# Kernel optimization log

Measured on AMD Instinct MI355X. Metric: run time of the kernel, lower is better.

Reference implementation:

```python
import jax, jax.numpy as jnp
import numpy as np

B, C, H, W = 2, 4, 256, 256   # x shape; H == W == num_classes
NH = 2                         # num_heads
NC = 256                       # num_classes
CT = C * 256                   # conv output channels (dim * 16 * 16)
NCR = NC // 16                 # MLP reduced dim


def setup_inputs() -> dict:
    key = jax.random.key(0)
    ks = jax.random.split(key, 16)
    s = 0.02

    def n(k, shape):
        return jax.random.normal(k, shape, jnp.float32) * s

    inp = {
        "x": jax.random.normal(ks[0], (B, C, H, W), jnp.float32),
        "conv_w": n(ks[1], (CT, C, 3, 3)),          # OIHW
        "conv_b": jnp.zeros((CT,), jnp.float32),
        # MLP weights stored (in, out) so y = x @ W + b  (== torch Linear)
        "qW1": n(ks[2], (NC, NCR)), "qb1": jnp.zeros((NCR,), jnp.float32),
        "qW2": n(ks[3], (NC, NCR)), "qb2": jnp.zeros((NCR,), jnp.float32),
        "kW1": n(ks[4], (NC, NCR)), "kb1": jnp.zeros((NCR,), jnp.float32),
        "kW2": n(ks[5], (NC, NCR)), "kb2": jnp.zeros((NCR,), jnp.float32),
        "vW1": n(ks[6], (NC, NCR)), "vb1": jnp.zeros((NCR,), jnp.float32),
        "vW2": n(ks[7], (NC, NCR)), "vb2": jnp.zeros((NCR,), jnp.float32),
        "temperature": jnp.ones((NH * NH, 1, 1), jnp.float32),
    }
    return inp


def _mlp(x, W1, b1, W2, b2):
    # Linear+sigmoid on last dim (w), transpose, Linear+sigmoid on (h), transpose back
    x = jax.nn.sigmoid(x @ W1 + b1)      # (b, ct, h, w//16)
    x = jnp.swapaxes(x, 2, 3)            # (b, ct, w//16, h)
    x = jax.nn.sigmoid(x @ W2 + b2)      # (b, ct, w//16, h//16)
    return jnp.swapaxes(x, 2, 3)         # (b, ct, h//16, w//16)


def _to_heads(a, nh):
    # einops: 'b c (h head1) (w head2) -> b (head1 head2) c (h w)'
    bb, ct, ht, wt = a.shape
    a = a.reshape(bb, ct, ht // nh, nh, wt // nh, nh)
    a = a.transpose(0, 3, 5, 1, 2, 4)    # (b, head1, head2, c, h, w)
    return a.reshape(bb, nh * nh, ct, (ht // nh) * (wt // nh))


def reference(x, conv_w, conv_b, qW1, qb1, qW2, qb2, kW1, kb1, kW2, kb2,
              vW1, vb1, vW2, vb2, temperature):
    b, c, h, w = x.shape
    t = jax.lax.conv_general_dilated(
        x, conv_w, window_strides=(1, 1), padding=((1, 1), (1, 1)),
        dimension_numbers=("NCHW", "OIHW", "NCHW")) + conv_b[None, :, None, None]
    q = _to_heads(_mlp(t, qW1, qb1, qW2, qb2), NH)   # (b, nh^2, ct, hw')
    k = _to_heads(_mlp(t, kW1, kb1, kW2, kb2), NH)
    v = _to_heads(_mlp(t, vW1, vb1, vW2, vb2), NH)
    scores = jnp.einsum('bncx,bnex->bnce', q, k) * temperature  # (b, nh^2, ct, ct)
    p = jax.nn.softmax(scores, axis=-1)
    att = jnp.einsum('bnce,bnex->bncx', p, v)                   # (b, nh^2, ct, hw')
    return att.reshape(b, c, h, w)
```

## Files before the change

### kernel.cpp

```cpp
#include <hip/hip_runtime.h>
#include <cstdint>

constexpr int NB  = 2;
constexpr int NCI = 4;
constexpr int NHH = 256;
constexpr int NWW = 256;
constexpr int NCT = 1024;

constexpr size_t SW1F = 0;
constexpr size_t U16_BASE_F = 48;
constexpr size_t GP_U  = 0;
constexpr size_t CW_U  = 297216;
constexpr size_t W2T_U = 338176;
constexpr size_t QU_O  = 350464;
constexpr size_t KU_O  = 874752;
constexpr size_t VT_O  = 1399040;

typedef __attribute__((ext_vector_type(8))) short bf16x8;
typedef __attribute__((ext_vector_type(4))) float f32x4;

__device__ __forceinline__ uint16_t f2bf(float x) {
  uint32_t u = __float_as_uint(x);
  return (uint16_t)((u + 0x7FFFu + ((u >> 16) & 1u)) >> 16);
}
__device__ __forceinline__ uint32_t pk2bf(float a, float b) {
  const uint32_t au = __float_as_uint(a) + 0x8000u;
  const uint32_t bu = __float_as_uint(b) + 0x8000u;
  return __builtin_amdgcn_perm(bu, au, 0x07060302u);
}
__device__ __forceinline__ float sigmoid_f(float v) {
  return __builtin_amdgcn_rcpf(1.0f + __expf(-v));
}

__global__ __launch_bounds__(64) void k1_G(
    const float* __restrict__ x,
    const float* __restrict__ qW1, const float* __restrict__ kW1,
    const float* __restrict__ vW1,
    const float* __restrict__ conv_w,
    const float* __restrict__ qW2, const float* __restrict__ kW2,
    const float* __restrict__ vW2,
    float* __restrict__ wsf, uint16_t* __restrict__ wsu) {
  const int tid = threadIdx.x;
  const int NBLK = 3 * NB * NCI * (NHH / 4);
  int bid = blockIdx.x;

  if (bid >= NBLK + 3 + 64) {
    const int p = bid - (NBLK + 3 + 64);
    const int m = p >> 3;
    const int h0 = (p & 7) * 32;
    const float* W2 = (m == 0) ? qW2 : (m == 1) ? kW2 : vW2;
    const int hh = tid >> 1, part = tid & 1;
    const float* src = W2 + (size_t)(h0 + hh) * 16 + part * 8;
    const float4 a = *(const float4*)(src);
    const float4 b2 = *(const float4*)(src + 4);
    uint16_t* dst = wsu + W2T_U + (size_t)m * 4096 + h0 + hh;
    dst[(part * 8 + 0) * 256] = f2bf(a.x);
    dst[(part * 8 + 1) * 256] = f2bf(a.y);
    dst[(part * 8 + 2) * 256] = f2bf(a.z);
    dst[(part * 8 + 3) * 256] = f2bf(a.w);
    dst[(part * 8 + 4) * 256] = f2bf(b2.x);
    dst[(part * 8 + 5) * 256] = f2bf(b2.y);
    dst[(part * 8 + 6) * 256] = f2bf(b2.z);
    dst[(part * 8 + 7) * 256] = f2bf(b2.w);
    return;
  }
  if (bid >= NBLK + 3) {
    const int p = bid - (NBLK + 3);
    const int o = p * 16 + (tid >> 2);
    const int ks = (tid & 3) * 10;
    for (int u = 0; u < 10; ++u) {
      const int k = ks + u;
      wsu[CW_U + (size_t)o * 40 + k] = (k < 36) ? f2bf(conv_w[o * 36 + k]) : (uint16_t)0;
    }
    return;
  }
  if (bid >= NBLK) {
    const int m = bid - NBLK;
    const float* W1 = (m == 0) ? qW1 : (m == 1) ? kW1 : vW1;
    const int wc = tid >> 4, r = tid & 15;
    float s = 0.f;
    #pragma unroll 8
    for (int i = 0; i < 64; ++i) s += W1[(wc * 64 + i) * 16 + r];
    s += __shfl_xor(s, 16, 64);
    s += __shfl_xor(s, 32, 64);
    if (tid < 16) wsf[SW1F + m * 16 + tid] = s;
    return;
  }

  const int m  = bid / (NB * NCI * (NHH / 4));
  int rem      = bid % (NB * NCI * (NHH / 4));
  const int b  = rem / (NCI * (NHH / 4));
  rem          = rem % (NCI * (NHH / 4));
  const int i  = rem / (NHH / 4);
  const int h0 = (rem % (NHH / 4)) * 4;
  const int mb = m * NB + b;

  const float* W1 = (m == 0) ? qW1 : (m == 1) ? kW1 : vW1;

  __shared__ float W1l[16 * 260];
  __shared__ float xlb[4][260];

  for (int idx4 = tid; idx4 < 1024; idx4 += 64) {
    const float4 t = ((const float4*)W1)[idx4];
    const int w = idx4 >> 2, r0 = (idx4 & 3) * 4;
    W1l[(r0 + 0) * 260 + w] = t.x;
    W1l[(r0 + 1) * 260 + w] = t.y;
    W1l[(r0 + 2) * 260 + w] = t.z;
    W1l[(r0 + 3) * 260 + w] = t.w;
  }
  const float* xbase = x + ((size_t)(b * NCI + i) * NHH + h0) * NWW;
  for (int idx = tid; idx < 4 * 256; idx += 64) {
    const int rr = idx >> 8, w = idx & 255;
    xlb[rr][1 + w] = xbase[rr * NWW + w];
  }
  if (tid < 4) {
    xlb[tid][0] = 0.f; xlb[tid][257] = 0.f; xlb[tid][258] = 0.f; xlb[tid][259] = 0.f;
  }
  __syncthreads();

  if (h0 == 0 && tid < 48) {
    const int dxp = tid >> 4, rp = tid & 15;
    wsu[GP_U + ((size_t)((mb * 4 + i) * 3 + dxp) * 16 + rp) * 258 + 0] = 0;
  }
  if (h0 == 252 && tid < 48) {
    const int dxp = tid >> 4, rp = tid & 15;
    wsu[GP_U + ((size_t)((mb * 4 + i) * 3 + dxp) * 16 + rp) * 258 + 257] = 0;
  }

  const int wc = tid >> 4, r = tid & 15;
  const int w0 = wc * 64;
  const size_t gb0 = GP_U + ((size_t)((mb * 4 + i) * 3 + 0) * 16 + r) * 258;

  #pragma unroll
  for (int rr = 0; rr < 4; ++rr) {
    const float* xl = xlb[rr];
    float a0 = 0.f, a1 = 0.f, a2 = 0.f;
    float4 cur = *(const float4*)&xl[w0];
    #pragma unroll 4
    for (int w = w0; w < w0 + 64; w += 4) {
      const float4 nxt = *(const float4*)&xl[w + 4];
      const float4 w1  = *(const float4*)&W1l[r * 260 + w];
      a0 += w1.x * cur.x + w1.y * cur.y + w1.z * cur.z + w1.w * cur.w;
      a1 += w1.x * cur.y + w1.y * cur.z + w1.z * cur.w + w1.w * nxt.x;
      a2 += w1.x * cur.z + w1.y * cur.w + w1.z * nxt.x + w1.w * nxt.y;
      cur = nxt;
    }
    a0 += __shfl_xor(a0, 16, 64); a0 += __shfl_xor(a0, 32, 64);
    a1 += __shfl_xor(a1, 16, 64); a1 += __shfl_xor(a1, 32, 64);
    a2 += __shfl_xor(a2, 16, 64); a2 += __shfl_xor(a2, 32, 64);
    if (wc == 0) {
      const int hp = 1 + h0 + rr;
      wsu[gb0 + hp]        = f2bf(a0);
      wsu[gb0 + 4128 + hp] = f2bf(a1);
      wsu[gb0 + 8256 + hp] = f2bf(a2);
    }
  }
}

__global__ __launch_bounds__(256, 4) void k2_mfma(
    const uint16_t* __restrict__ gp, const uint16_t* __restrict__ cwbf,
    const uint16_t* __restrict__ w2t,
    const float* __restrict__ conv_b,
    const float* __restrict__ qb1, const float* __restrict__ kb1, const float* __restrict__ vb1,
    const float* __restrict__ qb2, const float* __restrict__ kb2, const float* __restrict__ vb2,
    const float* __restrict__ wsf, uint16_t* __restrict__ wsu) {
  const int tid = threadIdx.x;
  const int bid = blockIdx.x;
  const int r  = bid & 15;
  const int og = (bid >> 4) & 15;
  const int mb = bid >> 8;
  const int m  = mb >> 1, b = mb & 1;

  const int wv  = tid >> 6;
  const int l   = tid & 63;
  const int l15 = l & 15;
  const int lg  = l >> 4;

  __shared__ uint16_t GS[256 * 40];
  __shared__ uint16_t y1l[4][16 * 72];

  {
    const int h = tid;
    uint16_t* gsrow = &GS[h * 40];
    #pragma unroll
    for (int i = 0; i < 4; ++i) {
      #pragma unroll
      for (int dx = 0; dx < 3; ++dx) {
        const uint16_t* g = gp + ((size_t)((mb * 4 + i) * 3 + dx) * 16 + r) * 258 + h;
        gsrow[i * 9 + 0 * 3 + dx] = g[0];
        gsrow[i * 9 + 1 * 3 + dx] = g[1];
        gsrow[i * 9 + 2 * 3 + dx] = g[2];
      }
    }
    gsrow[36] = 0; gsrow[37] = 0; gsrow[38] = 0; gsrow[39] = 0;
  }
  __syncthreads();

  const float* b1 = (m == 0) ? qb1 : (m == 1) ? kb1 : vb1;
  const float* b2 = (m == 0) ? qb2 : (m == 1) ? kb2 : vb2;

  const int o_blk = og * 64 + wv * 16;

  const uint16_t* cwrow = cwbf + (size_t)(o_blk + l15) * 40;
  bf16x8 cw0 = *(const bf16x8*)(cwrow + lg * 8);
  bf16x8 cw1 = {0,0,0,0,0,0,0,0};
  if (lg == 0) cw1 = *(const bf16x8*)(cwrow + 32);

  const uint16_t* w2row = w2t + (size_t)m * 4096 + (size_t)l15 * 256 + lg * 8;
  bf16x8 w2f0 = *(const bf16x8*)(w2row + 0 * 32);
  bf16x8 w2f1 = *(const bf16x8*)(w2row + 1 * 32);
  bf16x8 w2f2 = *(const bf16x8*)(w2row + 2 * 32);
  bf16x8 w2f3 = *(const bf16x8*)(w2row + 3 * 32);
  bf16x8 w2f4 = *(const bf16x8*)(w2row + 4 * 32);
  bf16x8 w2f5 = *(const bf16x8*)(w2row + 5 * 32);
  bf16x8 w2f6 = *(const bf16x8*)(w2row + 6 * 32);
  bf16x8 w2f7 = *(const bf16x8*)(w2row + 7 * 32);

  const float sw1r = wsf[SW1F + m * 16 + r];
  const float b1r  = b1[r];
  const float cbv  = conv_b[o_blk + l15];
  const float bias1 = cbv * sw1r + b1r;
  const float b2v  = b2[l15];

  uint16_t* yw = &y1l[wv][0];
  f32x4 acc2 = {0.f, 0.f, 0.f, 0.f};

  #pragma unroll
  for (int cc = 0; cc < 4; ++cc) {
    #pragma unroll
    for (int ct = 0; ct < 4; ++ct) {
      const uint16_t* arow = &GS[(cc * 64 + ct * 16 + l15) * 40];
      bf16x8 a0 = *(const bf16x8*)(arow + lg * 8);
      bf16x8 a1 = {0,0,0,0,0,0,0,0};
      if (lg == 0) a1 = *(const bf16x8*)(arow + 32);
      f32x4 d = {0.f, 0.f, 0.f, 0.f};
      d = __builtin_amdgcn_mfma_f32_16x16x32_bf16(a0, cw0, d, 0, 0, 0);
      d = __builtin_amdgcn_mfma_f32_16x16x32_bf16(a1, cw1, d, 0, 0, 0);
      const float y0 = sigmoid_f(d[0] + bias1);
      const float y1 = sigmoid_f(d[1] + bias1);
      const float y2 = sigmoid_f(d[2] + bias1);
      const float y3 = sigmoid_f(d[3] + bias1);
      uint32_t* yd = (uint32_t*)&yw[l15 * 72 + ct * 16 + lg * 4];
      yd[0] = pk2bf(y0, y1);
      yd[1] = pk2bf(y2, y3);
    }
    {
      const uint16_t* yrow = &yw[l15 * 72 + lg * 8];
      bf16x8 ya0 = *(const bf16x8*)(yrow + 0);
      bf16x8 ya1 = *(const bf16x8*)(yrow + 32);
      if (cc == 0) {
        acc2 = __builtin_amdgcn_mfma_f32_16x16x32_bf16(ya0, w2f0, acc2, 0, 0, 0);
        acc2 = __builtin_amdgcn_mfma_f32_16x16x32_bf16(ya1, w2f1, acc2, 0, 0, 0);
      } else if (cc == 1) {
        acc2 = __builtin_amdgcn_mfma_f32_16x16x32_bf16(ya0, w2f2, acc2, 0, 0, 0);
        acc2 = __builtin_amdgcn_mfma_f32_16x16x32_bf16(ya1, w2f3, acc2, 0, 0, 0);
      } else if (cc == 2) {
        acc2 = __builtin_amdgcn_mfma_f32_16x16x32_bf16(ya0, w2f4, acc2, 0, 0, 0);
        acc2 = __builtin_amdgcn_mfma_f32_16x16x32_bf16(ya1, w2f5, acc2, 0, 0, 0);
      } else {
        acc2 = __builtin_amdgcn_mfma_f32_16x16x32_bf16(ya0, w2f6, acc2, 0, 0, 0);
        acc2 = __builtin_amdgcn_mfma_f32_16x16x32_bf16(ya1, w2f7, acc2, 0, 0, 0);
      }
    }
  }

  const int s   = l15;
  const int n   = (s & 1) * 2 + (r & 1);
  const int xsp = (s >> 1) * 8 + (r >> 1);
  const int bn  = b * 4 + n;
  uint16_t* qk = wsu + ((m == 0) ? QU_O : KU_O);
  uint16_t* vT = wsu + VT_O;
  #pragma unroll
  for (int p = 0; p < 4; ++p) {
    const int o = o_blk + lg * 4 + p;
    const uint16_t y2 = f2bf(sigmoid_f(acc2[p] + b2v));
    if (m == 2) vT[((size_t)bn * 64 + xsp) * 1024 + o] = y2;
    else        qk[((size_t)bn * 1024 + o) * 64 + xsp] = y2;
  }
}

__global__ __launch_bounds__(512, 4) void k3_attn(
    const uint16_t* __restrict__ qu, const uint16_t* __restrict__ ku,
    const uint16_t* __restrict__ vtu, const float* __restrict__ temp,
    float* __restrict__ out) {
  const int tid = threadIdx.x;
  const int wv  = tid >> 6;
  const int l   = tid & 63;
  const int l15 = l & 15, lg = l >> 4;
  const int bid = blockIdx.x;
  const int bn = bid & 7;
  const int ct = bid >> 3;
  const int cbase = ct * 16;
  const float tsc2 = temp[bn & 3] * 1.44269504089f;

  __shared__ __align__(16) char SH[36864];
  uint16_t* pl  = (uint16_t*)SH + wv * 2304;
  float* poS = (float*)SH;
  float* mlS = poS + 8704;

  const uint16_t* qrow = qu + (size_t)(bn * 1024 + cbase + l15) * 64 + lg * 8;
  const bf16x8 qf0 = *(const bf16x8*)(qrow);
  const bf16x8 qf1 = *(const bf16x8*)(qrow + 32);

  const uint16_t* kb = ku  + (size_t)bn * 65536 + lg * 8;
  const uint16_t* vb = vtu + (size_t)bn * 65536 + lg * 8;

  f32x4 o0 = {0.f,0.f,0.f,0.f}, o1 = o0, o2 = o0, o3 = o0;
  float mrun = -1.0e30f, lrun = 0.f;

  #pragma unroll
  for (int t = 0; t < 2; ++t) {
    const int e0 = wv * 128 + t * 64;

    const uint16_t* kr0 = kb + (size_t)(e0 +  0 + l15) * 64;
    const uint16_t* kr1 = kb + (size_t)(e0 + 16 + l15) * 64;
    const uint16_t* kr2 = kb + (size_t)(e0 + 32 + l15) * 64;
    const uint16_t* kr3 = kb + (size_t)(e0 + 48 + l15) * 64;
    const bf16x8 ka0 = *(const bf16x8*)(kr0);
    const bf16x8 kb0 = *(const bf16x8*)(kr0 + 32);
    const bf16x8 ka1 = *(const bf16x8*)(kr1);
    const bf16x8 kb1_ = *(const bf16x8*)(kr1 + 32);
    const bf16x8 ka2 = *(const bf16x8*)(kr2);
    const bf16x8 kb2_ = *(const bf16x8*)(kr2 + 32);
    const bf16x8 ka3 = *(const bf16x8*)(kr3);
    const bf16x8 kb3_ = *(const bf16x8*)(kr3 + 32);

    f32x4 s0 = {0.f,0.f,0.f,0.f}, s1 = s0, s2 = s0, s3 = s0;
    s0 = __builtin_amdgcn_mfma_f32_16x16x32_bf16(ka0, qf0, s0, 0,0,0);
    s0 = __builtin_amdgcn_mfma_f32_16x16x32_bf16(kb0, qf1, s0, 0,0,0);
    s1 = __builtin_amdgcn_mfma_f32_16x16x32_bf16(ka1, qf0, s1, 0,0,0);
    s1 = __builtin_amdgcn_mfma_f32_16x16x32_bf16(kb1_, qf1, s1, 0,0,0);
    s2 = __builtin_amdgcn_mfma_f32_16x16x32_bf16(ka2, qf0, s2, 0,0,0);
    s2 = __builtin_amdgcn_mfma_f32_16x16x32_bf16(kb2_, qf1, s2, 0,0,0);
    s3 = __builtin_amdgcn_mfma_f32_16x16x32_bf16(ka3, qf0, s3, 0,0,0);
    s3 = __builtin_amdgcn_mfma_f32_16x16x32_bf16(kb3_, qf1, s3, 0,0,0);

    const uint16_t* vr0 = vb + (size_t)( 0 + l15) * 1024 + e0;
    const uint16_t* vr1 = vb + (size_t)(16 + l15) * 1024 + e0;
    const uint16_t* vr2 = vb + (size_t)(32 + l15) * 1024 + e0;
    const uint16_t* vr3 = vb + (size_t)(48 + l15) * 1024 + e0;
    const bf16x8 v0a = *(const bf16x8*)(vr0);
    const bf16x8 v0b = *(const bf16x8*)(vr0 + 32);
    const bf16x8 v1a = *(const bf16x8*)(vr1);
    const bf16x8 v1b = *(const bf16x8*)(vr1 + 32);
    const bf16x8 v2a = *(const bf16x8*)(vr2);
    const bf16x8 v2b = *(const bf16x8*)(vr2 + 32);
    const bf16x8 v3a = *(const bf16x8*)(vr3);
    const bf16x8 v3b = *(const bf16x8*)(vr3 + 32);

    #pragma unroll
    for (int p = 0; p < 4; ++p) {
      s0[p] *= tsc2; s1[p] *= tsc2; s2[p] *= tsc2; s3[p] *= tsc2;
    }
    float t0 = fmaxf(fmaxf(s0[0], s0[1]), fmaxf(s0[2], s0[3]));
    float t1 = fmaxf(fmaxf(s1[0], s1[1]), fmaxf(s1[2], s1[3]));
    float t2 = fmaxf(fmaxf(s2[0], s2[1]), fmaxf(s2[2], s2[3]));
    float t3 = fmaxf(fmaxf(s3[0], s3[1]), fmaxf(s3[2], s3[3]));
    float tmax = fmaxf(fmaxf(t0, t1), fmaxf(t2, t3));
    tmax = fmaxf(tmax, __shfl_xor(tmax, 16, 64));
    tmax = fmaxf(tmax, __shfl_xor(tmax, 32, 64));
    const float mnew = fmaxf(mrun, tmax);
    const float scl  = exp2f(mrun - mnew);
    float psum = 0.f;
    #pragma unroll
    for (int p = 0; p < 4; ++p) { s0[p] = exp2f(s0[p] - mnew); psum += s0[p]; }
    #pragma unroll
    for (int p = 0; p < 4; ++p) { s1[p] = exp2f(s1[p] - mnew); psum += s1[p]; }
    #pragma unroll
    for (int p = 0; p < 4; ++p) { s2[p] = exp2f(s2[p] - mnew); psum += s2[p]; }
    #pragma unroll
    for (int p = 0; p < 4; ++p) { s3[p] = exp2f(s3[p] - mnew); psum += s3[p]; }
    psum += __shfl_xor(psum, 16, 64);
    psum += __shfl_xor(psum, 32, 64);
    lrun = lrun * scl + psum;
    mrun = mnew;

    {
      uint32_t* p0w = (uint32_t*)&pl[l15 * 72 +  0 + lg * 4];
      uint32_t* p1w = (uint32_t*)&pl[l15 * 72 + 16 + lg * 4];
      uint32_t* p2w = (uint32_t*)&pl[l15 * 72 + 32 + lg * 4];
      uint32_t* p3w = (uint32_t*)&pl[l15 * 72 + 48 + lg * 4];
      p0w[0] = pk2bf(s0[0], s0[1]); p0w[1] = pk2bf(s0[2], s0[3]);
      p1w[0] = pk2bf(s1[0], s1[1]); p1w[1] = pk2bf(s1[2], s1[3]);
      p2w[0] = pk2bf(s2[0], s2[1]); p2w[1] = pk2bf(s2[2], s2[3]);
      p3w[0] = pk2bf(s3[0], s3[1]); p3w[1] = pk2bf(s3[2], s3[3]);
    }

    #pragma unroll
    for (int p = 0; p < 4; ++p) {
      o0[p] *= scl; o1[p] *= scl; o2[p] *= scl; o3[p] *= scl;
    }

    {
      const bf16x8 pb0 = *(const bf16x8*)&pl[l15 * 72 +  0 + lg * 8];
      const bf16x8 pb1 = *(const bf16x8*)&pl[l15 * 72 + 32 + lg * 8];
      o0 = __builtin_amdgcn_mfma_f32_16x16x32_bf16(v0a, pb0, o0, 0,0,0);
      o0 = __builtin_amdgcn_mfma_f32_16x16x32_bf16(v0b, pb1, o0, 0,0,0);
      o1 = __builtin_amdgcn_mfma_f32_16x16x32_bf16(v1a, pb0, o1, 0,0,0);
      o1 = __builtin_amdgcn_mfma_f32_16x16x32_bf16(v1b, pb1, o1, 0,0,0);
      o2 = __builtin_amdgcn_mfma_f32_16x16x32_bf16(v2a, pb0, o2, 0,0,0);
      o2 = __builtin_amdgcn_mfma_f32_16x16x32_bf16(v2b, pb1, o2, 0,0,0);
      o3 = __builtin_amdgcn_mfma_f32_16x16x32_bf16(v3a, pb0, o3, 0,0,0);
      o3 = __builtin_amdgcn_mfma_f32_16x16x32_bf16(v3b, pb1, o3, 0,0,0);
    }
  }

  __syncthreads();

  {
    float* po = poS + wv * 1088 + l15 * 68 + lg * 4;
    *(f32x4*)&po[ 0] = o0;
    *(f32x4*)&po[16] = o1;
    *(f32x4*)&po[32] = o2;
    *(f32x4*)&po[48] = o3;
    if (lg == 0) {
      mlS[wv * 32 + l15]      = mrun;
      mlS[wv * 32 + 16 + l15] = lrun;
    }
  }
  __syncthreads();

  {
    const int c  = tid >> 5;
    const int x2 = (tid & 31) * 2;

    float m0 = mlS[0 * 32 + c], m1 = mlS[1 * 32 + c];
    float m2 = mlS[2 * 32 + c], m3 = mlS[3 * 32 + c];
    float m4 = mlS[4 * 32 + c], m5 = mlS[5 * 32 + c];
    float m6 = mlS[6 * 32 + c], m7 = mlS[7 * 32 + c];
    const float M = fmaxf(fmaxf(fmaxf(m0, m1), fmaxf(m2, m3)),
                          fmaxf(fmaxf(m4, m5), fmaxf(m6, m7)));
    const float c0 = exp2f(m0 - M), c1 = exp2f(m1 - M);
    const float c2 = exp2f(m2 - M), c3 = exp2f(m3 - M);
    const float c4 = exp2f(m4 - M), c5 = exp2f(m5 - M);
    const float c6 = exp2f(m6 - M), c7 = exp2f(m7 - M);
    const float L = c0 * mlS[0 * 32 + 16 + c] + c1 * mlS[1 * 32 + 16 + c]
                  + c2 * mlS[2 * 32 + 16 + c] + c3 * mlS[3 * 32 + 16 + c]
                  + c4 * mlS[4 * 32 + 16 + c] + c5 * mlS[5 * 32 + 16 + c]
                  + c6 * mlS[6 * 32 + 16 + c] + c7 * mlS[7 * 32 + 16 + c];
    const float rl = __builtin_amdgcn_rcpf(L);

    const float* pb = poS + c * 68 + x2;
    float a0 = 0.f, a1 = 0.f;
    a0 += c0 * pb[0 * 1088]; a1 += c0 * pb[0 * 1088 + 1];
    a0 += c1 * pb[1 * 1088]; a1 += c1 * pb[1 * 1088 + 1];
    a0 += c2 * pb[2 * 1088]; a1 += c2 * pb[2 * 1088 + 1];
    a0 += c3 * pb[3 * 1088]; a1 += c3 * pb[3 * 1088 + 1];
    a0 += c4 * pb[4 * 1088]; a1 += c4 * pb[4 * 1088 + 1];
    a0 += c5 * pb[5 * 1088]; a1 += c5 * pb[5 * 1088 + 1];
    a0 += c6 * pb[6 * 1088]; a1 += c6 * pb[6 * 1088 + 1];
    a0 += c7 * pb[7 * 1088]; a1 += c7 * pb[7 * 1088 + 1];

    const int C = cbase + c;
    float* ob = out + ((size_t)bn * 256 + (C >> 2)) * 256 + (C & 3) * 64 + x2;
    ob[0] = a0 * rl;
    ob[1] = a1 * rl;
  }
}

extern "C" void kernel_launch(void* const* d_in, const int* in_sizes, int n_in,
                              void* d_out, int out_size, void* d_ws, size_t ws_size,
                              hipStream_t stream) {
  (void)in_sizes; (void)n_in; (void)out_size; (void)ws_size;
  const float* x      = (const float*)d_in[0];
  const float* conv_w = (const float*)d_in[1];
  const float* conv_b = (const float*)d_in[2];
  const float* qW1 = (const float*)d_in[3];
  const float* qb1 = (const float*)d_in[4];
  const float* qW2 = (const float*)d_in[5];
  const float* qb2 = (const float*)d_in[6];
  const float* kW1 = (const float*)d_in[7];
  const float* kb1 = (const float*)d_in[8];
  const float* kW2 = (const float*)d_in[9];
  const float* kb2 = (const float*)d_in[10];
  const float* vW1 = (const float*)d_in[11];
  const float* vb1 = (const float*)d_in[12];
  const float* vW2 = (const float*)d_in[13];
  const float* vb2 = (const float*)d_in[14];
  const float* temp = (const float*)d_in[15];
  float* wsf = (float*)d_ws;
  uint16_t* wsu = (uint16_t*)(wsf + U16_BASE_F);
  float* out = (float*)d_out;

  k1_G<<<dim3(1627), dim3(64), 0, stream>>>(x, qW1, kW1, vW1,
      conv_w, qW2, kW2, vW2, wsf, wsu);
  k2_mfma<<<dim3(1536), dim3(256), 0, stream>>>(
      wsu + GP_U, wsu + CW_U, wsu + W2T_U, conv_b,
      qb1, kb1, vb1, qb2, kb2, vb2, wsf, wsu);
  k3_attn<<<dim3(512), dim3(512), 0, stream>>>(
      wsu + QU_O, wsu + KU_O, wsu + VT_O, temp, out);
}
```

Before: 47.66 us.

## Process two 16-row query tiles per attention block to reuse K/V loads

The attention kernel now has each block handle 32 query channels (two 16-row tiles) instead of 16. Each wave reuses its loaded K and V fragments for both tiles and keeps two independent online-softmax states, which halves global K/V traffic per output and halves the grid to 256 blocks. The cost is more registers and LDS (about 70KB), launch bounds lowered to 2 blocks per CU, and fewer blocks to fill the GPU's CUs. The final cross-wave merge is rewritten to emit four outputs per thread.

Result: faster. 41.65 us (-12.6%).

```diff
diff --git a/kernel.cpp b/kernel.cpp
--- a/kernel.cpp
+++ b/kernel.cpp
@@ -279,7 +279,7 @@
   }
 }
 
-__global__ __launch_bounds__(512, 4) void k3_attn(
+__global__ __launch_bounds__(512, 2) void k3_attn(
     const uint16_t* __restrict__ qu, const uint16_t* __restrict__ ku,
     const uint16_t* __restrict__ vtu, const float* __restrict__ temp,
     float* __restrict__ out) {
@@ -289,24 +289,30 @@
   const int l15 = l & 15, lg = l >> 4;
   const int bid = blockIdx.x;
   const int bn = bid & 7;
-  const int ct = bid >> 3;
-  const int cbase = ct * 16;
+  const int cg = bid >> 3;
+  const int cbase = cg * 32;
   const float tsc2 = temp[bn & 3] * 1.44269504089f;
 
-  __shared__ __align__(16) char SH[36864];
-  uint16_t* pl  = (uint16_t*)SH + wv * 2304;
+  __shared__ __align__(16) char SH[71680];
+  uint16_t* plA = (uint16_t*)SH + (wv * 2 + 0) * 1152;
+  uint16_t* plB = (uint16_t*)SH + (wv * 2 + 1) * 1152;
   float* poS = (float*)SH;
-  float* mlS = poS + 8704;
-
-  const uint16_t* qrow = qu + (size_t)(bn * 1024 + cbase + l15) * 64 + lg * 8;
-  const bf16x8 qf0 = *(const bf16x8*)(qrow);
-  const bf16x8 qf1 = *(const bf16x8*)(qrow + 32);
+  float* mlS = poS + 17408;
+
+  const uint16_t* qrowA = qu + (size_t)(bn * 1024 + cbase + l15) * 64 + lg * 8;
+  const uint16_t* qrowB = qrowA + 16 * 64;
+  const bf16x8 qf0a = *(const bf16x8*)(qrowA);
+  const bf16x8 qf1a = *(const bf16x8*)(qrowA + 32);
+  const bf16x8 qf0b = *(const bf16x8*)(qrowB);
+  const bf16x8 qf1b = *(const bf16x8*)(qrowB + 32);
 
   const uint16_t* kb = ku  + (size_t)bn * 65536 + lg * 8;
   const uint16_t* vb = vtu + (size_t)bn * 65536 + lg * 8;
 
-  f32x4 o0 = {0.f,0.f,0.f,0.f}, o1 = o0, o2 = o0, o3 = o0;
-  float mrun = -1.0e30f, lrun = 0.f;
+  f32x4 oa0 = {0.f,0.f,0.f,0.f}, oa1 = oa0, oa2 = oa0, oa3 = oa0;
+  f32x4 ob0 = oa0, ob1 = oa0, ob2 = oa0, ob3 = oa0;
+  float mrunA = -1.0e30f, lrunA = 0.f;
+  float mrunB = -1.0e30f, lrunB = 0.f;
 
   #pragma unroll
   for (int t = 0; t < 2; ++t) {
@@ -326,14 +332,23 @@
     const bf16x8 kb3_ = *(const bf16x8*)(kr3 + 32);
 
     f32x4 s0 = {0.f,0.f,0.f,0.f}, s1 = s0, s2 = s0, s3 = s0;
-    s0 = __builtin_amdgcn_mfma_f32_16x16x32_bf16(ka0, qf0, s0, 0,0,0);
-    s0 = __builtin_amdgcn_mfma_f32_16x16x32_bf16(kb0, qf1, s0, 0,0,0);
-    s1 = __builtin_amdgcn_mfma_f32_16x16x32_bf16(ka1, qf0, s1, 0,0,0);
-    s1 = __builtin_amdgcn_mfma_f32_16x16x32_bf16(kb1_, qf1, s1, 0,0,0);
-    s2 = __builtin_amdgcn_mfma_f32_16x16x32_bf16(ka2, qf0, s2, 0,0,0);
-    s2 = __builtin_amdgcn_mfma_f32_16x16x32_bf16(kb2_, qf1, s2, 0,0,0);
-    s3 = __builtin_amdgcn_mfma_f32_16x16x32_bf16(ka3, qf0, s3, 0,0,0);
-    s3 = __builtin_amdgcn_mfma_f32_16x16x32_bf16(kb3_, qf1, s3, 0,0,0);
+    f32x4 u0 = s0, u1 = s0, u2 = s0, u3 = s0;
+    s0 = __builtin_amdgcn_mfma_f32_16x16x32_bf16(ka0, qf0a, s0, 0,0,0);
+    s0 = __builtin_amdgcn_mfma_f32_16x16x32_bf16(kb0, qf1a, s0, 0,0,0);
+    s1 = __builtin_amdgcn_mfma_f32_16x16x32_bf16(ka1, qf0a, s1, 0,0,0);
+    s1 = __builtin_amdgcn_mfma_f32_16x16x32_bf16(kb1_, qf1a, s1, 0,0,0);
+    s2 = __builtin_amdgcn_mfma_f32_16x16x32_bf16(ka2, qf0a, s2, 0,0,0);
+    s2 = __builtin_amdgcn_mfma_f32_16x16x32_bf16(kb2_, qf1a, s2, 0,0,0);
+    s3 = __builtin_amdgcn_mfma_f32_16x16x32_bf16(ka3, qf0a, s3, 0,0,0);
+    s3 = __builtin_amdgcn_mfma_f32_16x16x32_bf16(kb3_, qf1a, s3, 0,0,0);
+    u0 = __builtin_amdgcn_mfma_f32_16x16x32_bf16(ka0, qf0b, u0, 0,0,0);
+    u0 = __builtin_amdgcn_mfma_f32_16x16x32_bf16(kb0, qf1b, u0, 0,0,0);
+    u1 = __builtin_amdgcn_mfma_f32_16x16x32_bf16(ka1, qf0b, u1, 0,0,0);
+    u1 = __builtin_amdgcn_mfma_f32_16x16x32_bf16(kb1_, qf1b, u1, 0,0,0);
+    u2 = __builtin_amdgcn_mfma_f32_16x16x32_bf16(ka2, qf0b, u2, 0,0,0);
+    u2 = __builtin_amdgcn_mfma_f32_16x16x32_bf16(kb2_, qf1b, u2, 0,0,0);
+    u3 = __builtin_amdgcn_mfma_f32_16x16x32_bf16(ka3, qf0b, u3, 0,0,0);
+    u3 = __builtin_amdgcn_mfma_f32_16x16x32_bf16(kb3_, qf1b, u3, 0,0,0);
 
     const uint16_t* vr0 = vb + (size_t)( 0 + l15) * 1024 + e0;
     const uint16_t* vr1 = vb + (size_t)(16 + l15) * 1024 + e0;
@@ -348,113 +363,167 @@
     const bf16x8 v3a = *(const bf16x8*)(vr3);
     const bf16x8 v3b = *(const bf16x8*)(vr3 + 32);
 
-    #pragma unroll
-    for (int p = 0; p < 4; ++p) {
-      s0[p] *= tsc2; s1[p] *= tsc2; s2[p] *= tsc2; s3[p] *= tsc2;
-    }
-    float t0 = fmaxf(fmaxf(s0[0], s0[1]), fmaxf(s0[2], s0[3]));
-    float t1 = fmaxf(fmaxf(s1[0], s1[1]), fmaxf(s1[2], s1[3]));
-    float t2 = fmaxf(fmaxf(s2[0], s2[1]), fmaxf(s2[2], s2[3]));
-    float t3 = fmaxf(fmaxf(s3[0], s3[1]), fmaxf(s3[2], s3[3]));
-    float tmax = fmaxf(fmaxf(t0, t1), fmaxf(t2, t3));
-    tmax = fmaxf(tmax, __shfl_xor(tmax, 16, 64));
-    tmax = fmaxf(tmax, __shfl_xor(tmax, 32, 64));
-    const float mnew = fmaxf(mrun, tmax);
-    const float scl  = exp2f(mrun - mnew);
-    float psum = 0.f;
-    #pragma unroll
-    for (int p = 0; p < 4; ++p) { s0[p] = exp2f(s0[p] - mnew); psum += s0[p]; }
-    #pragma unroll
-    for (int p = 0; p < 4; ++p) { s1[p] = exp2f(s1[p] - mnew); psum += s1[p]; }
-    #pragma unroll
-    for (int p = 0; p < 4; ++p) { s2[p] = exp2f(s2[p] - mnew); psum += s2[p]; }
-    #pragma unroll
-    for (int p = 0; p < 4; ++p) { s3[p] = exp2f(s3[p] - mnew); psum += s3[p]; }
-    psum += __shfl_xor(psum, 16, 64);
-    psum += __shfl_xor(psum, 32, 64);
-    lrun = lrun * scl + psum;
-    mrun = mnew;
-
     {
-      uint32_t* p0w = (uint32_t*)&pl[l15 * 72 +  0 + lg * 4];
-      uint32_t* p1w = (uint32_t*)&pl[l15 * 72 + 16 + lg * 4];
-      uint32_t* p2w = (uint32_t*)&pl[l15 * 72 + 32 + lg * 4];
-      uint32_t* p3w = (uint32_t*)&pl[l15 * 72 + 48 + lg * 4];
+      #pragma unroll
+      for (int p = 0; p < 4; ++p) {
+        s0[p] *= tsc2; s1[p] *= tsc2; s2[p] *= tsc2; s3[p] *= tsc2;
+      }
+      float t0 = fmaxf(fmaxf(s0[0], s0[1]), fmaxf(s0[2], s0[3]));
+      float t1 = fmaxf(fmaxf(s1[0], s1[1]), fmaxf(s1[2], s1[3]));
+      float t2 = fmaxf(fmaxf(s2[0], s2[1]), fmaxf(s2[2], s2[3]));
+      float t3 = fmaxf(fmaxf(s3[0], s3[1]), fmaxf(s3[2], s3[3]));
+      float tmax = fmaxf(fmaxf(t0, t1), fmaxf(t2, t3));
+      tmax = fmaxf(tmax, __shfl_xor(tmax, 16, 64));
+      tmax = fmaxf(tmax, __shfl_xor(tmax, 32, 64));
+      const float mnew = fmaxf(mrunA, tmax);
+      const float scl  = exp2f(mrunA - mnew);
+      float psum = 0.f;
+      #pragma unroll
+      for (int p = 0; p < 4; ++p) { s0[p] = exp2f(s0[p] - mnew); psum += s0[p]; }
+      #pragma unroll
+      for (int p = 0; p < 4; ++p) { s1[p] = exp2f(s1[p] - mnew); psum += s1[p]; }
+      #pragma unroll
+      for (int p = 0; p < 4; ++p) { s2[p] = exp2f(s2[p] - mnew); psum += s2[p]; }
+      #pragma unroll
+      for (int p = 0; p < 4; ++p) { s3[p] = exp2f(s3[p] - mnew); psum += s3[p]; }
+      psum += __shfl_xor(psum, 16, 64);
+      psum += __shfl_xor(psum, 32, 64);
+      lrunA = lrunA * scl + psum;
+      mrunA = mnew;
+      uint32_t* p0w = (uint32_t*)&plA[l15 * 72 +  0 + lg * 4];
+      uint32_t* p1w = (uint32_t*)&plA[l15 * 72 + 16 + lg * 4];
+      uint32_t* p2w = (uint32_t*)&plA[l15 * 72 + 32 + lg * 4];
+      uint32_t* p3w = (uint32_t*)&plA[l15 * 72 + 48 + lg * 4];
       p0w[0] = pk2bf(s0[0], s0[1]); p0w[1] = pk2bf(s0[2], s0[3]);
       p1w[0] = pk2bf(s1[0], s1[1]); p1w[1] = pk2bf(s1[2], s1[3]);
       p2w[0] = pk2bf(s2[0], s2[1]); p2w[1] = pk2bf(s2[2], s2[3]);
       p3w[0] = pk2bf(s3[0], s3[1]); p3w[1] = pk2bf(s3[2], s3[3]);
-    }
-
+      #pragma unroll
+      for (int p = 0; p < 4; ++p) {
+        oa0[p] *= scl; oa1[p] *= scl; oa2[p] *= scl; oa3[p] *= scl;
+      }
+    }
+    {
+      #pragma unroll
+      for (int p = 0; p < 4; ++p) {
+        u0[p] *= tsc2; u1[p] *= tsc2; u2[p] *= tsc2; u3[p] *= tsc2;
+      }
+      float t0 = fmaxf(fmaxf(u0[0], u0[1]), fmaxf(u0[2], u0[3]));
+      float t1 = fmaxf(fmaxf(u1[0], u1[1]), fmaxf(u1[2], u1[3]));
+      float t2 = fmaxf(fmaxf(u2[0], u2[1]), fmaxf(u2[2], u2[3]));
+      float t3 = fmaxf(fmaxf(u3[0], u3[1]), fmaxf(u3[2], u3[3]));
+      float tmax = fmaxf(fmaxf(t0, t1), fmaxf(t2, t3));
+      tmax = fmaxf(tmax, __shfl_xor(tmax, 16, 64));
+      tmax = fmaxf(tmax, __shfl_xor(tmax, 32, 64));
+      const float mnew = fmaxf(mrunB, tmax);
+      const float scl  = exp2f(mrunB - mnew);
+      float psum = 0.f;
+      #pragma unroll
+      for (int p = 0; p < 4; ++p) { u0[p] = exp2f(u0[p] - mnew); psum += u0[p]; }
+      #pragma unroll
+      for (int p = 0; p < 4; ++p) { u1[p] = exp2f(u1[p] - mnew); psum += u1[p]; }
+      #pragma unroll
+      for (int p = 0; p < 4; ++p) { u2[p] = exp2f(u2[p] - mnew); psum += u2[p]; }
+      #pragma unroll
+      for (int p = 0; p < 4; ++p) { u3[p] = exp2f(u3[p] - mnew); psum += u3[p]; }
+      psum += __shfl_xor(psum, 16, 64);
+      psum += __shfl_xor(psum, 32, 64);
+      lrunB = lrunB * scl + psum;
+      mrunB = mnew;
+      uint32_t* p0w = (uint32_t*)&plB[l15 * 72 +  0 + lg * 4];
+      uint32_t* p1w = (uint32_t*)&plB[l15 * 72 + 16 + lg * 4];
+      uint32_t* p2w = (uint32_t*)&plB[l15 * 72 + 32 + lg * 4];
+      uint32_t* p3w = (uint32_t*)&plB[l15 * 72 + 48 + lg * 4];
+      p0w[0] = pk2bf(u0[0], u0[1]); p0w[1] = pk2bf(u0[2], u0[3]);
+      p1w[0] = pk2bf(u1[0], u1[1]); p1w[1] = pk2bf(u1[2], u1[3]);
+      p2w[0] = pk2bf(u2[0], u2[1]); p2w[1] = pk2bf(u2[2], u2[3]);
+      p3w[0] = pk2bf(u3[0], u3[1]); p3w[1] = pk2bf(u3[2], u3[3]);
+      #pragma unroll
+      for (int p = 0; p < 4; ++p) {
+        ob0[p] *= scl; ob1[p] *= scl; ob2[p] *= scl; ob3[p] *= scl;
+      }
+    }
+
+    {
+      const bf16x8 pa0 = *(const bf16x8*)&plA[l15 * 72 +  0 + lg * 8];
+      const bf16x8 pa1 = *(const bf16x8*)&plA[l15 * 72 + 32 + lg * 8];
+      const bf16x8 pb0 = *(const bf16x8*)&plB[l15 * 72 +  0 + lg * 8];
+      const bf16x8 pb1 = *(const bf16x8*)&plB[l15 * 72 + 32 + lg * 8];
+      oa0 = __builtin_amdgcn_mfma_f32_16x16x32_bf16(v0a, pa0, oa0, 0,0,0);
+      oa0 = __builtin_amdgcn_mfma_f32_16x16x32_bf16(v0b, pa1, oa0, 0,0,0);
+      oa1 = __builtin_amdgcn_mfma_f32_16x16x32_bf16(v1a, pa0, oa1, 0,0,0);
+      oa1 = __builtin_amdgcn_mfma_f32_16x16x32_bf16(v1b, pa1, oa1, 0,0,0);
+      oa2 = __builtin_amdgcn_mfma_f32_16x16x32_bf16(v2a, pa0, oa2, 0,0,0);
+      oa2 = __builtin_amdgcn_mfma_f32_16x16x32_bf16(v2b, pa1, oa2, 0,0,0);
+      oa3 = __builtin_amdgcn_mfma_f32_16x16x32_bf16(v3a, pa0, oa3, 0,0,0);
+      oa3 = __builtin_amdgcn_mfma_f32_16x16x32_bf16(v3b, pa1, oa3, 0,0,0);
+      ob0 = __builtin_amdgcn_mfma_f32_16x16x32_bf16(v0a, pb0, ob0, 0,0,0);
+      ob0 = __builtin_amdgcn_mfma_f32_16x16x32_bf16(v0b, pb1, ob0, 0,0,0);
+      ob1 = __builtin_amdgcn_mfma_f32_16x16x32_bf16(v1a, pb0, ob1, 0,0,0);
+      ob1 = __builtin_amdgcn_mfma_f32_16x16x32_bf16(v1b, pb1, ob1, 0,0,0);
+      ob2 = __builtin_amdgcn_mfma_f32_16x16x32_bf16(v2a, pb0, ob2, 0,0,0);
+      ob2 = __builtin_amdgcn_mfma_f32_16x16x32_bf16(v2b, pb1, ob2, 0,0,0);
+      ob3 = __builtin_amdgcn_mfma_f32_16x16x32_bf16(v3a, pb0, ob3, 0,0,0);
+      ob3 = __builtin_amdgcn_mfma_f32_16x16x32_bf16(v3b, pb1, ob3, 0,0,0);
+    }
+  }
+
+  __syncthreads();
+
+  {
+    float* poA = poS + (wv * 2 + 0) * 1088 + l15 * 68 + lg * 4;
+    float* poB = poS + (wv * 2 + 1) * 1088 + l15 * 68 + lg * 4;
+    *(f32x4*)&poA[ 0] = oa0;
+    *(f32x4*)&poA[16] = oa1;
+    *(f32x4*)&poA[32] = oa2;
+    *(f32x4*)&poA[48] = oa3;
+    *(f32x4*)&poB[ 0] = ob0;
+    *(f32x4*)&poB[16] = ob1;
+    *(f32x4*)&poB[32] = ob2;
+    *(f32x4*)&poB[48] = ob3;
+    if (lg == 0) {
+      mlS[(wv * 2 + 0) * 32 + l15]      = mrunA;
+      mlS[(wv * 2 + 0) * 32 + 16 + l15] = lrunA;
+      mlS[(wv * 2 + 1) * 32 + l15]      = mrunB;
+      mlS[(wv * 2 + 1) * 32 + 16 + l15] = lrunB;
+    }
+  }
+  __syncthreads();
+
+  {
+    const int c  = tid >> 4;
+    const int x4 = (tid & 15) * 4;
+    const int ctile = c >> 4, cl = c & 15;
+
+    float mj[8], lj[8];
     #pragma unroll
-    for (int p = 0; p < 4; ++p) {
-      o0[p] *= scl; o1[p] *= scl; o2[p] *= scl; o3[p] *= scl;
-    }
-
-    {
-      const bf16x8 pb0 = *(const bf16x8*)&pl[l15 * 72 +  0 + lg * 8];
-      const bf16x8 pb1 = *(const bf16x8*)&pl[l15 * 72 + 32 + lg * 8];
-      o0 = __builtin_amdgcn_mfma_f32_16x16x32_bf16(v0a, pb0, o0, 0,0,0);
-      o0 = __builtin_amdgcn_mfma_f32_16x16x32_bf16(v0b, pb1, o0, 0,0,0);
-      o1 = __builtin_amdgcn_mfma_f32_16x16x32_bf16(v1a, pb0, o1, 0,0,0);
-      o1 = __builtin_amdgcn_mfma_f32_16x16x32_bf16(v1b, pb1, o1, 0,0,0);
-      o2 = __builtin_amdgcn_mfma_f32_16x16x32_bf16(v2a, pb0, o2, 0,0,0);
-      o2 = __builtin_amdgcn_mfma_f32_16x16x32_bf16(v2b, pb1, o2, 0,0,0);
-      o3 = __builtin_amdgcn_mfma_f32_16x16x32_bf16(v3a, pb0, o3, 0,0,0);
-      o3 = __builtin_amdgcn_mfma_f32_16x16x32_bf16(v3b, pb1, o3, 0,0,0);
-    }
-  }
-
-  __syncthreads();
-
-  {
-    float* po = poS + wv * 1088 + l15 * 68 + lg * 4;
-    *(f32x4*)&po[ 0] = o0;
-    *(f32x4*)&po[16] = o1;
-    *(f32x4*)&po[32] = o2;
-    *(f32x4*)&po[48] = o3;
-    if (lg == 0) {
-      mlS[wv * 32 + l15]      = mrun;
-      mlS[wv * 32 + 16 + l15] = lrun;
-    }
-  }
-  __syncthreads();
-
-  {
-    const int c  = tid >> 5;
-    const int x2 = (tid & 31) * 2;
-
-    float m0 = mlS[0 * 32 + c], m1 = mlS[1 * 32 + c];
-    float m2 = mlS[2 * 32 + c], m3 = mlS[3 * 32 + c];
-    float m4 = mlS[4 * 32 + c], m5 = mlS[5 * 32 + c];
-    float m6 = mlS[6 * 32 + c], m7 = mlS[7 * 32 + c];
-    const float M = fmaxf(fmaxf(fmaxf(m0, m1), fmaxf(m2, m3)),
-                          fmaxf(fmaxf(m4, m5), fmaxf(m6, m7)));
-    const float c0 = exp2f(m0 - M), c1 = exp2f(m1 - M);
-    const float c2 = exp2f(m2 - M), c3 = exp2f(m3 - M);
-    const float c4 = exp2f(m4 - M), c5 = exp2f(m5 - M);
-    const float c6 = exp2f(m6 - M), c7 = exp2f(m7 - M);
-    const float L = c0 * mlS[0 * 32 + 16 + c] + c1 * mlS[1 * 32 + 16 + c]
-                  + c2 * mlS[2 * 32 + 16 + c] + c3 * mlS[3 * 32 + 16 + c]
-                  + c4 * mlS[4 * 32 + 16 + c] + c5 * mlS[5 * 32 + 16 + c]
-                  + c6 * mlS[6 * 32 + 16 + c] + c7 * mlS[7 * 32 + 16 + c];
+    for (int j = 0; j < 8; ++j) {
+      mj[j] = mlS[(j * 2 + ctile) * 32 + cl];
+      lj[j] = mlS[(j * 2 + ctile) * 32 + 16 + cl];
+    }
+    float M = mj[0];
+    #pragma unroll
+    for (int j = 1; j < 8; ++j) M = fmaxf(M, mj[j]);
+    float cj[8];
+    float L = 0.f;
+    #pragma unroll
+    for (int j = 0; j < 8; ++j) { cj[j] = exp2f(mj[j] - M); L += cj[j] * lj[j]; }
     const float rl = __builtin_amdgcn_rcpf(L);
 
-    const float* pb = poS + c * 68 + x2;
-    float a0 = 0.f, a1 = 0.f;
-    a0 += c0 * pb[0 * 1088]; a1 += c0 * pb[0 * 1088 + 1];
-    a0 += c1 * pb[1 * 1088]; a1 += c1 * pb[1 * 1088 + 1];
-    a0 += c2 * pb[2 * 1088]; a1 += c2 * pb[2 * 1088 + 1];
-    a0 += c3 * pb[3 * 1088]; a1 += c3 * pb[3 * 1088 + 1];
-    a0 += c4 * pb[4 * 1088]; a1 += c4 * pb[4 * 1088 + 1];
-    a0 += c5 * pb[5 * 1088]; a1 += c5 * pb[5 * 1088 + 1];
-    a0 += c6 * pb[6 * 1088]; a1 += c6 * pb[6 * 1088 + 1];
-    a0 += c7 * pb[7 * 1088]; a1 += c7 * pb[7 * 1088 + 1];
+    float a0 = 0.f, a1 = 0.f, a2 = 0.f, a3 = 0.f;
+    #pragma unroll
+    for (int j = 0; j < 8; ++j) {
+      const f32x4 pv = *(const f32x4*)&poS[(j * 2 + ctile) * 1088 + cl * 68 + x4];
+      a0 += cj[j] * pv[0]; a1 += cj[j] * pv[1];
+      a2 += cj[j] * pv[2]; a3 += cj[j] * pv[3];
+    }
 
     const int C = cbase + c;
-    float* ob = out + ((size_t)bn * 256 + (C >> 2)) * 256 + (C & 3) * 64 + x2;
+    float* ob = out + ((size_t)bn * 256 + (C >> 2)) * 256 + (C & 3) * 64 + x4;
     ob[0] = a0 * rl;
     ob[1] = a1 * rl;
+    ob[2] = a2 * rl;
+    ob[3] = a3 * rl;
   }
 }
 
@@ -487,6 +556,6 @@
   k2_mfma<<<dim3(1536), dim3(256), 0, stream>>>(
       wsu + GP_U, wsu + CW_U, wsu + W2T_U, conv_b,
       qb1, kb1, vb1, qb2, kb2, vb2, wsf, wsu);
-  k3_attn<<<dim3(512), dim3(512), 0, stream>>>(
+  k3_attn<<<dim3(256), dim3(512), 0, stream>>>(
       wsu + QU_O, wsu + KU_O, wsu + VT_O, temp, out);
 }
```
